# Performance work log

Measured on AMD Instinct MI355X. Metric: run time of the kernel, lower is better.

The kernel has to match this reference:

```python
import jax, jax.numpy as jnp
import numpy as np

B, S, I, H, C = 256, 128, 512, 1024, 10
VOCAB = S  # nn.Embedding(seq_length, input_dim)


def _lstm_dir(embeds_tbi, W, b):
    """Run an LSTM over time. embeds_tbi: [S,B,I]; W: [4H, I+H] stacked (g,i,f,o); b: [4H]."""
    h0 = jnp.zeros((B, H), jnp.float32)
    c0 = jnp.zeros((B, H), jnp.float32)

    def step(carry, x_t):
        c, h = carry
        xh = jnp.concatenate([x_t, h], axis=1)          # [B, I+H]
        z = xh @ W.T + b                                 # [B, 4H]
        g, i, f, o = jnp.split(z, 4, axis=1)
        g = jnp.tanh(g)
        i = jax.nn.sigmoid(i)
        f = jax.nn.sigmoid(f)
        o = jax.nn.sigmoid(o)
        new_c = g * i + c * f
        new_h = jnp.tanh(new_c) * o
        return (new_c, new_h), None

    (c_T, h_T), _ = jax.lax.scan(step, (c0, h0), embeds_tbi)
    return h_T


def setup_inputs() -> dict:
    key = jax.random.key(0)
    ks = jax.random.split(key, 8)
    x = jax.random.randint(ks[0], (B, S), 0, VOCAB)
    embed = jax.random.normal(ks[1], (VOCAB, I), jnp.float32) * 0.5
    scale = 1.0 / np.sqrt(I + H)
    fwd_W = jax.random.normal(ks[2], (4 * H, I + H), jnp.float32) * scale  # stacked g,i,f,o
    fwd_b = jax.random.normal(ks[3], (4 * H,), jnp.float32) * 0.02
    bwd_W = jax.random.normal(ks[4], (4 * H, I + H), jnp.float32) * scale
    bwd_b = jax.random.normal(ks[5], (4 * H,), jnp.float32) * 0.02
    p_w = jax.random.normal(ks[6], (C, 2 * H), jnp.float32) * (1.0 / np.sqrt(2 * H))
    p_b = jax.random.normal(ks[7], (C,), jnp.float32) * 0.02
    return {"x": x, "embed": embed, "fwd_W": fwd_W, "fwd_b": fwd_b,
            "bwd_W": bwd_W, "bwd_b": bwd_b, "p_w": p_w, "p_b": p_b}


def reference(x, embed, fwd_W, fwd_b, bwd_W, bwd_b, p_w, p_b):
    embeds = embed[x]                       # [B,S,I]
    emb_t = jnp.transpose(embeds, (1, 0, 2))  # [S,B,I]
    h_fwd = _lstm_dir(emb_t, fwd_W, fwd_b)
    h_bwd = _lstm_dir(emb_t[::-1], bwd_W, bwd_b)
    h_comb = jnp.concatenate([h_fwd, h_bwd], axis=1)  # [B,2H]
    return jax.nn.log_softmax(h_comb @ p_w.T + p_b, axis=1)
```

## Files before the change

### kernel.cpp

```cpp
#include <hip/hip_runtime.h>
#include <hip/hip_bf16.h>
#include <math.h>

#define B 256
#define S 128
#define I_DIM 512
#define H 1024
#define C 10
#define WROW 1536

#define LDS_H 131072

typedef float f32x4 __attribute__((ext_vector_type(4), may_alias));
typedef __bf16 bf16x8 __attribute__((ext_vector_type(8), may_alias));
typedef unsigned int u32x4 __attribute__((ext_vector_type(4), may_alias));
typedef unsigned long long u64;
typedef unsigned long long __attribute__((may_alias)) u64a;

__device__ __forceinline__ unsigned short f2bf(float f) {
    union { float f; unsigned u; } a; a.f = f;
    return (unsigned short)((a.u + 0x7fffu + ((a.u >> 16) & 1u)) >> 16);
}
__device__ __forceinline__ float bf2f(unsigned short b) {
    union { unsigned u; float f; } a; a.u = ((unsigned)b) << 16;
    return a.f;
}
__device__ __forceinline__ float sigf(float v) { return 1.0f / (1.0f + __expf(-v)); }
__device__ __forceinline__ float tanh_fast(float v) { return 1.0f - 2.0f / (1.0f + __expf(2.0f * v)); }

__global__ void wf_build(const float* __restrict__ fwd_W,
                         const float* __restrict__ bwd_W,
                         __hip_bfloat16* __restrict__ wF) {
    int gid = blockIdx.x * 256 + threadIdx.x;
    int lane = gid & 63, kk = (gid >> 6) & 31, nsub = (gid >> 11) & 255, d = gid >> 19;
    int n_gl = nsub * 16 + (lane & 15);
    int j = n_gl >> 2, g = n_gl & 3;
    int k = kk * 32 + (lane >> 4) * 8;
    const float* W = d ? bwd_W : fwd_W;
    const float* src = W + (size_t)(g * 1024 + j) * WROW + I_DIM + k;
    ushort4 lo = make_ushort4(f2bf(src[0]), f2bf(src[1]), f2bf(src[2]), f2bf(src[3]));
    ushort4 hi = make_ushort4(f2bf(src[4]), f2bf(src[5]), f2bf(src[6]), f2bf(src[7]));
    ushort4* dst = (ushort4*)(wF + (size_t)gid * 8);
    dst[0] = lo; dst[1] = hi;
}

__global__ void wxf_build(const float* __restrict__ fwd_W,
                          const float* __restrict__ bwd_W,
                          __hip_bfloat16* __restrict__ wxF) {
    int gid = blockIdx.x * 256 + threadIdx.x;
    int lane = gid & 63, kk = (gid >> 6) & 15, nsub = (gid >> 10) & 255, d = gid >> 18;
    int n_gl = nsub * 16 + (lane & 15);
    int j = n_gl >> 2, g = n_gl & 3;
    int k = kk * 32 + (lane >> 4) * 8;
    const float* W = d ? bwd_W : fwd_W;
    const float* src = W + (size_t)(g * 1024 + j) * WROW + k;
    ushort4 lo = make_ushort4(f2bf(src[0]), f2bf(src[1]), f2bf(src[2]), f2bf(src[3]));
    ushort4 hi = make_ushort4(f2bf(src[4]), f2bf(src[5]), f2bf(src[6]), f2bf(src[7]));
    ushort4* dst = (ushort4*)(wxF + (size_t)gid * 8);
    dst[0] = lo; dst[1] = hi;
}

__global__ void ehl_build(const float* __restrict__ embed,
                          unsigned short* __restrict__ ehl) {
    int idx = blockIdx.x * 256 + threadIdx.x;
    float e = embed[idx];
    unsigned short hb = f2bf(e);
    unsigned short lb = f2bf(e - bf2f(hb));
    ehl[idx] = hb;
    ehl[65536 + idx] = lb;
}

__global__ __launch_bounds__(256) void projp_mfma(
        const __hip_bfloat16* __restrict__ wxF,
        const unsigned short* __restrict__ ehl,
        const float* __restrict__ fwd_b,
        const float* __restrict__ bwd_b,
        float* __restrict__ projP) {
    extern __shared__ char sm[];
    const int bid = blockIdx.x;
    const int d = bid >> 7, jt = (bid >> 2) & 31, vb = bid & 3;
    const int tid = threadIdx.x, w = tid >> 6, lane = tid & 63;
    const int l15 = lane & 15, l4 = lane >> 4;
    const int v0 = vb * 32;

    for (int i = 0; i < 16; i++) {
        int chunk = i * 256 + tid;
        int row = chunk >> 6, c16 = chunk & 63;
        int p = row >> 5, vs = v0 + (row & 31);
        u32x4 vd = *(const u32x4*)(ehl + ((size_t)p * 128 + vs) * 512 + c16 * 8);
        *(u32x4*)(sm + row * 1024 + ((c16 * 16) ^ ((row & 7) << 4))) = vd;
    }
    __syncthreads();

    const __hip_bfloat16* ap0 = wxF + ((size_t)((d * 256 + jt * 8 + w * 2 + 0) * 16)) * 512;
    const __hip_bfloat16* ap1 = wxF + ((size_t)((d * 256 + jt * 8 + w * 2 + 1) * 16)) * 512;
    int hrow[2], hswz[2], lrow[2], lswz[2];
#pragma unroll
    for (int vt = 0; vt < 2; vt++) {
        int hr = vt * 16 + l15, lr = hr + 32;
        hrow[vt] = hr * 1024; hswz[vt] = (hr & 7) << 4;
        lrow[vt] = lr * 1024; lswz[vt] = (lr & 7) << 4;
    }
    f32x4 acc[2][2] = {};
#pragma unroll
    for (int kk = 0; kk < 16; kk++) {
        bf16x8 A0 = *(const bf16x8*)(ap0 + kk * 512 + lane * 8);
        bf16x8 A1 = *(const bf16x8*)(ap1 + kk * 512 + lane * 8);
        int ko = kk * 64 + l4 * 16;
        bf16x8 Bh0 = *(const bf16x8*)(sm + hrow[0] + (ko ^ hswz[0]));
        bf16x8 Bh1 = *(const bf16x8*)(sm + hrow[1] + (ko ^ hswz[1]));
        bf16x8 Bl0 = *(const bf16x8*)(sm + lrow[0] + (ko ^ lswz[0]));
        bf16x8 Bl1 = *(const bf16x8*)(sm + lrow[1] + (ko ^ lswz[1]));
        acc[0][0] = __builtin_amdgcn_mfma_f32_16x16x32_bf16(A0, Bh0, acc[0][0], 0, 0, 0);
        acc[0][0] = __builtin_amdgcn_mfma_f32_16x16x32_bf16(A0, Bl0, acc[0][0], 0, 0, 0);
        acc[0][1] = __builtin_amdgcn_mfma_f32_16x16x32_bf16(A0, Bh1, acc[0][1], 0, 0, 0);
        acc[0][1] = __builtin_amdgcn_mfma_f32_16x16x32_bf16(A0, Bl1, acc[0][1], 0, 0, 0);
        acc[1][0] = __builtin_amdgcn_mfma_f32_16x16x32_bf16(A1, Bh0, acc[1][0], 0, 0, 0);
        acc[1][0] = __builtin_amdgcn_mfma_f32_16x16x32_bf16(A1, Bl0, acc[1][0], 0, 0, 0);
        acc[1][1] = __builtin_amdgcn_mfma_f32_16x16x32_bf16(A1, Bh1, acc[1][1], 0, 0, 0);
        acc[1][1] = __builtin_amdgcn_mfma_f32_16x16x32_bf16(A1, Bl1, acc[1][1], 0, 0, 0);
    }
    const float* bp = d ? bwd_b : fwd_b;
#pragma unroll
    for (int nt = 0; nt < 2; nt++) {
        int j = jt * 32 + w * 8 + nt * 4 + l4;
        f32x4 bv = { bp[j], bp[1024 + j], bp[2048 + j], bp[3072 + j] };
#pragma unroll
        for (int vt = 0; vt < 2; vt++) {
            int v = v0 + vt * 16 + l15;
            *(f32x4*)(projP + ((size_t)(d * 1024 + j) * 128 + v) * 4) = acc[nt][vt] + bv;
        }
    }
}

__global__ __launch_bounds__(512, 1) void step_kernel(
        const int* __restrict__ x,
        const __hip_bfloat16* __restrict__ wF,
        const float* __restrict__ projP,
        __hip_bfloat16* __restrict__ hbuf,
        float* __restrict__ cws,
        int t) {
    extern __shared__ char smem[];
    const int bid = blockIdx.x;
    const int d = bid >> 7, bt = (bid >> 5) & 3, jt = bid & 31;
    const int tid = threadIdx.x, wid = tid >> 6, lane = tid & 63;
    const int l15 = lane & 15, l4 = lane >> 4;
    const int b0 = bt * 64;
    const size_t dBH = (size_t)d * B * H;

    const __hip_bfloat16* wp = wF + (size_t)(d * 256 + jt * 8 + wid) * 16384;

    bf16x8 Ap[8];
    if (t > 0) {
#pragma unroll
        for (int p = 0; p < 8; p++)
            Ap[p] = *(const bf16x8*)(wp + p * 512 + lane * 8);
    }
    const int tt = d ? (S - 1 - t) : t;
    int vv[4];
#pragma unroll
    for (int bs = 0; bs < 4; bs++)
        vv[bs] = x[(b0 + bs * 16 + l15) * S + tt];

    u32x4 sb1[8], sb2[8];
    int srow[8], sc16[8];
    if (t > 0) {
        const __hip_bfloat16* hr = hbuf + (size_t)(t & 1) * 2 * B * H + dBH + (size_t)b0 * H;
#pragma unroll
        for (int i = 0; i < 8; i++) {
            int flat = i * 512 + tid;
            srow[i] = flat >> 6;
            sc16[i] = flat & 63;
            sb1[i] = *(const u32x4*)(hr + (size_t)srow[i] * H + sc16[i] * 8);
        }
#pragma unroll
        for (int i = 0; i < 8; i++)
            sb2[i] = *(const u32x4*)(hr + (size_t)srow[i] * H + (sc16[i] + 64) * 8);
    }

    const int j = jt * 32 + wid * 4 + l4;
    const f32x4* pp = (const f32x4*)projP + ((size_t)d * 1024 + j) * 128;
    f32x4 pj[4];
#pragma unroll
    for (int bs = 0; bs < 4; bs++) pj[bs] = pp[vv[bs]];

    float* cp = cws + ((size_t)bid * 512 + tid) * 4;
    f32x4 cv = {0.f, 0.f, 0.f, 0.f};
    if (t > 0) cv = *(const f32x4*)cp;

    f32x4 acc[4] = {};
    if (t > 0) {
#pragma unroll
        for (int i = 0; i < 8; i++)
            *(u32x4*)(smem + srow[i] * 2048 + ((sc16[i] * 16) ^ ((srow[i] & 7) << 4))) = sb1[i];
        __syncthreads();

        int brow[4], bswz[4];
#pragma unroll
        for (int bs = 0; bs < 4; bs++) {
            int row = bs * 16 + l15;
            brow[bs] = row * 2048;
            bswz[bs] = (row & 7) << 4;
        }

#pragma unroll
        for (int kk = 0; kk < 16; kk++) {
            bf16x8 A = Ap[kk & 7];
            Ap[kk & 7] = *(const bf16x8*)(wp + (kk + 8) * 512 + lane * 8);
            int koff = kk * 64 + l4 * 16;
            bf16x8 B0 = *(const bf16x8*)(smem + brow[0] + (koff ^ bswz[0]));
            bf16x8 B1 = *(const bf16x8*)(smem + brow[1] + (koff ^ bswz[1]));
            bf16x8 B2 = *(const bf16x8*)(smem + brow[2] + (koff ^ bswz[2]));
            bf16x8 B3 = *(const bf16x8*)(smem + brow[3] + (koff ^ bswz[3]));
            acc[0] = __builtin_amdgcn_mfma_f32_16x16x32_bf16(A, B0, acc[0], 0, 0, 0);
            acc[1] = __builtin_amdgcn_mfma_f32_16x16x32_bf16(A, B1, acc[1], 0, 0, 0);
            acc[2] = __builtin_amdgcn_mfma_f32_16x16x32_bf16(A, B2, acc[2], 0, 0, 0);
            acc[3] = __builtin_amdgcn_mfma_f32_16x16x32_bf16(A, B3, acc[3], 0, 0, 0);
        }

#pragma unroll
        for (int i = 0; i < 8; i++)
            *(u32x4*)(smem + srow[i] * 2048 + (((sc16[i] + 64) * 16) ^ ((srow[i] & 7) << 4))) = sb2[i];
        __syncthreads();

#pragma unroll
        for (int kk = 16; kk < 32; kk++) {
            bf16x8 A = Ap[kk & 7];
            if (kk < 24)
                Ap[kk & 7] = *(const bf16x8*)(wp + (kk + 8) * 512 + lane * 8);
            int koff = kk * 64 + l4 * 16;
            bf16x8 B0 = *(const bf16x8*)(smem + brow[0] + (koff ^ bswz[0]));
            bf16x8 B1 = *(const bf16x8*)(smem + brow[1] + (koff ^ bswz[1]));
            bf16x8 B2 = *(const bf16x8*)(smem + brow[2] + (koff ^ bswz[2]));
            bf16x8 B3 = *(const bf16x8*)(smem + brow[3] + (koff ^ bswz[3]));
            acc[0] = __builtin_amdgcn_mfma_f32_16x16x32_bf16(A, B0, acc[0], 0, 0, 0);
            acc[1] = __builtin_amdgcn_mfma_f32_16x16x32_bf16(A, B1, acc[1], 0, 0, 0);
            acc[2] = __builtin_amdgcn_mfma_f32_16x16x32_bf16(A, B2, acc[2], 0, 0, 0);
            acc[3] = __builtin_amdgcn_mfma_f32_16x16x32_bf16(A, B3, acc[3], 0, 0, 0);
        }
    }

    float hnv[4];
#pragma unroll
    for (int bs = 0; bs < 4; bs++) {
        float zg = acc[bs][0] + pj[bs][0];
        float zi = acc[bs][1] + pj[bs][1];
        float zf = acc[bs][2] + pj[bs][2];
        float zo = acc[bs][3] + pj[bs][3];
        float gg = tanh_fast(zg);
        float ii = sigf(zi);
        float ff = sigf(zf);
        float oo = sigf(zo);
        float cn = gg * ii + cv[bs] * ff;
        cv[bs] = cn;
        hnv[bs] = tanh_fast(cn) * oo;
    }
    *(f32x4*)cp = cv;

    unsigned plo = (unsigned)f2bf(hnv[0]) | ((unsigned)f2bf(hnv[1]) << 16);
    unsigned phi = (unsigned)f2bf(hnv[2]) | ((unsigned)f2bf(hnv[3]) << 16);
    unsigned short o4[4];
#pragma unroll
    for (int p = 0; p < 4; p++) {
        int src = p * 16 + l15;
        unsigned vlo = __shfl(plo, src);
        unsigned vhi = __shfl(phi, src);
        unsigned sel = (l4 < 2) ? vlo : vhi;
        o4[p] = (l4 & 1) ? (unsigned short)(sel >> 16) : (unsigned short)(sel & 0xffffu);
    }
    u64 hv = (u64)o4[0] | ((u64)o4[1] << 16) | ((u64)o4[2] << 32) | ((u64)o4[3] << 48);
    __hip_bfloat16* hw = hbuf + (size_t)((t + 1) & 1) * 2 * B * H + dBH
                         + (size_t)(b0 + lane) * H + jt * 32 + wid * 4;
    *(u64a*)hw = hv;
}

__global__ void head_kernel(const __hip_bfloat16* __restrict__ hbuf,
                            const float* __restrict__ p_w,
                            const float* __restrict__ p_b,
                            float* __restrict__ out) {
    int b = blockIdx.x;
    int lane = threadIdx.x;
    float part[C];
#pragma unroll
    for (int cc = 0; cc < C; cc++) part[cc] = 0.0f;
    for (int jj = lane; jj < 2 * H; jj += 64) {
        float hv = (jj < H)
            ? __bfloat162float(hbuf[(size_t)b * H + jj])
            : __bfloat162float(hbuf[(size_t)B * H + (size_t)b * H + jj - H]);
#pragma unroll
        for (int cc = 0; cc < C; cc++) part[cc] += hv * p_w[cc * 2 * H + jj];
    }
#pragma unroll
    for (int cc = 0; cc < C; cc++) {
        float v = part[cc];
        for (int off = 32; off; off >>= 1) v += __shfl_down(v, off);
        part[cc] = v;
    }
    if (lane == 0) {
        float lg[C];
        float m = -1e30f;
        for (int cc = 0; cc < C; cc++) {
            lg[cc] = part[cc] + p_b[cc];
            m = fmaxf(m, lg[cc]);
        }
        float s = 0.0f;
        for (int cc = 0; cc < C; cc++) s += expf(lg[cc] - m);
        float lse = logf(s) + m;
        for (int cc = 0; cc < C; cc++) out[b * C + cc] = lg[cc] - lse;
    }
}

extern "C" void kernel_launch(void* const* d_in, const int* in_sizes, int n_in,
                              void* d_out, int out_size, void* d_ws, size_t ws_size,
                              hipStream_t stream) {
    const int*   x     = (const int*)d_in[0];
    const float* embed = (const float*)d_in[1];
    const float* fwd_W = (const float*)d_in[2];
    const float* fwd_b = (const float*)d_in[3];
    const float* bwd_W = (const float*)d_in[4];
    const float* bwd_b = (const float*)d_in[5];
    const float* p_w   = (const float*)d_in[6];
    const float* p_b   = (const float*)d_in[7];
    float* outp = (float*)d_out;

    char* ws = (char*)d_ws;
    __hip_bfloat16* wF  = (__hip_bfloat16*)ws;  ws += (size_t)2 * 256 * 16384 * 2;
    __hip_bfloat16* wxF = (__hip_bfloat16*)ws;
    float* cws = (float*)ws;                    ws += (size_t)2 * 256 * 8192 * 2;
    unsigned short* ehl = (unsigned short*)ws;  ws += (size_t)2 * 128 * 512 * 2;
    float* projP = (float*)ws;                  ws += (size_t)2 * 1024 * 128 * 4 * 4;
    __hip_bfloat16* hbuf = (__hip_bfloat16*)ws; ws += (size_t)2 * 2 * B * H * 2;

    hipLaunchKernelGGL(wf_build, dim3(4096), dim3(256), 0, stream, fwd_W, bwd_W, wF);
    hipLaunchKernelGGL(wxf_build, dim3(2048), dim3(256), 0, stream, fwd_W, bwd_W, wxF);
    hipLaunchKernelGGL(ehl_build, dim3(256), dim3(256), 0, stream, embed, ehl);

    hipFuncSetAttribute((const void*)projp_mfma,
                        hipFuncAttributeMaxDynamicSharedMemorySize, 65536);
    hipLaunchKernelGGL(projp_mfma, dim3(256), dim3(256), 65536, stream,
                       wxF, ehl, fwd_b, bwd_b, projP);

    hipFuncSetAttribute((const void*)step_kernel,
                        hipFuncAttributeMaxDynamicSharedMemorySize, LDS_H);
    for (int t = 0; t < S; t++)
        hipLaunchKernelGGL(step_kernel, dim3(256), dim3(512), LDS_H, stream,
                           x, wF, projP, hbuf, cws, t);

    hipLaunchKernelGGL(head_kernel, dim3(B), dim3(64), 0, stream,
                       hbuf, p_w, p_b, outp);
}
```

Baseline: 1.648 ms.

## Switch recurrent step to 32x32x16 MFMA with single-pass LDS staging

```diff
diff --git a/kernel.cpp b/kernel.cpp
--- a/kernel.cpp
+++ b/kernel.cpp
@@ -12,6 +12,7 @@
 #define LDS_H 131072
 
 typedef float f32x4 __attribute__((ext_vector_type(4), may_alias));
+typedef float f32x16 __attribute__((ext_vector_type(16), may_alias));
 typedef __bf16 bf16x8 __attribute__((ext_vector_type(8), may_alias));
 typedef unsigned int u32x4 __attribute__((ext_vector_type(4), may_alias));
 typedef unsigned long long u64;
@@ -28,14 +29,14 @@
 __device__ __forceinline__ float sigf(float v) { return 1.0f / (1.0f + __expf(-v)); }
 __device__ __forceinline__ float tanh_fast(float v) { return 1.0f - 2.0f / (1.0f + __expf(2.0f * v)); }
 
-__global__ void wf_build(const float* __restrict__ fwd_W,
-                         const float* __restrict__ bwd_W,
-                         __hip_bfloat16* __restrict__ wF) {
+__global__ void wf_build32(const float* __restrict__ fwd_W,
+                           const float* __restrict__ bwd_W,
+                           __hip_bfloat16* __restrict__ wF) {
     int gid = blockIdx.x * 256 + threadIdx.x;
-    int lane = gid & 63, kk = (gid >> 6) & 31, nsub = (gid >> 11) & 255, d = gid >> 19;
-    int n_gl = nsub * 16 + (lane & 15);
+    int lane = gid & 63, kstep = (gid >> 6) & 63, nsub = (gid >> 12) & 127, d = gid >> 19;
+    int n_gl = nsub * 32 + (lane & 31);
     int j = n_gl >> 2, g = n_gl & 3;
-    int k = kk * 32 + (lane >> 4) * 8;
+    int k = kstep * 16 + (lane >> 5) * 8;
     const float* W = d ? bwd_W : fwd_W;
     const float* src = W + (size_t)(g * 1024 + j) * WROW + I_DIM + k;
     ushort4 lo = make_ushort4(f2bf(src[0]), f2bf(src[1]), f2bf(src[2]), f2bf(src[3]));
@@ -144,11 +145,12 @@
     const int bid = blockIdx.x;
     const int d = bid >> 7, bt = (bid >> 5) & 3, jt = bid & 31;
     const int tid = threadIdx.x, wid = tid >> 6, lane = tid & 63;
-    const int l15 = lane & 15, l4 = lane >> 4;
+    const int ngrp = wid >> 1, bgrp = wid & 1;
+    const int l31 = lane & 31, l32 = lane >> 5;
     const int b0 = bt * 64;
     const size_t dBH = (size_t)d * B * H;
 
-    const __hip_bfloat16* wp = wF + (size_t)(d * 256 + jt * 8 + wid) * 16384;
+    const __hip_bfloat16* wp = wF + (size_t)(d * 128 + jt * 4 + ngrp) * 32768;
 
     bf16x8 Ap[8];
     if (t > 0) {
@@ -157,120 +159,79 @@
             Ap[p] = *(const bf16x8*)(wp + p * 512 + lane * 8);
     }
     const int tt = d ? (S - 1 - t) : t;
-    int vv[4];
-#pragma unroll
-    for (int bs = 0; bs < 4; bs++)
-        vv[bs] = x[(b0 + bs * 16 + l15) * S + tt];
-
-    u32x4 sb1[8], sb2[8];
-    int srow[8], sc16[8];
-    if (t > 0) {
-        const __hip_bfloat16* hr = hbuf + (size_t)(t & 1) * 2 * B * H + dBH + (size_t)b0 * H;
-#pragma unroll
-        for (int i = 0; i < 8; i++) {
-            int flat = i * 512 + tid;
-            srow[i] = flat >> 6;
-            sc16[i] = flat & 63;
-            sb1[i] = *(const u32x4*)(hr + (size_t)srow[i] * H + sc16[i] * 8);
-        }
-#pragma unroll
-        for (int i = 0; i < 8; i++)
-            sb2[i] = *(const u32x4*)(hr + (size_t)srow[i] * H + (sc16[i] + 64) * 8);
-    }
-
-    const int j = jt * 32 + wid * 4 + l4;
-    const f32x4* pp = (const f32x4*)projP + ((size_t)d * 1024 + j) * 128;
-    f32x4 pj[4];
-#pragma unroll
-    for (int bs = 0; bs < 4; bs++) pj[bs] = pp[vv[bs]];
+    const int bg = b0 + bgrp * 32 + l31;
+    const int vv = x[bg * S + tt];
 
     float* cp = cws + ((size_t)bid * 512 + tid) * 4;
     f32x4 cv = {0.f, 0.f, 0.f, 0.f};
     if (t > 0) cv = *(const f32x4*)cp;
 
-    f32x4 acc[4] = {};
     if (t > 0) {
-#pragma unroll
-        for (int i = 0; i < 8; i++)
-            *(u32x4*)(smem + srow[i] * 2048 + ((sc16[i] * 16) ^ ((srow[i] & 7) << 4))) = sb1[i];
+        const __hip_bfloat16* hr = hbuf + (size_t)(t & 1) * 2 * B * H + dBH + (size_t)b0 * H;
+#pragma unroll
+        for (int i = 0; i < 16; i++) {
+            int flat = i * 512 + tid;
+            int row = flat >> 7, c16 = flat & 127;
+            u32x4 v = *(const u32x4*)(hr + (size_t)row * H + c16 * 8);
+            *(u32x4*)(smem + row * 2048 + ((c16 * 16) ^ ((row & 7) << 4))) = v;
+        }
+    }
+
+    f32x4 pj[4];
+#pragma unroll
+    for (int p = 0; p < 4; p++) {
+        int j = jt * 32 + ngrp * 8 + 2 * p + l32;
+        pj[p] = *((const f32x4*)projP + ((size_t)(d * 1024 + j) * 128 + vv));
+    }
+
+    f32x16 acc = {};
+    if (t > 0) {
         __syncthreads();
-
-        int brow[4], bswz[4];
-#pragma unroll
-        for (int bs = 0; bs < 4; bs++) {
-            int row = bs * 16 + l15;
-            brow[bs] = row * 2048;
-            bswz[bs] = (row & 7) << 4;
+        const int brow = (bgrp * 32 + l31) * 2048;
+        const int bswz = (l31 & 7) << 4;
+        bf16x8 Bp[4];
+#pragma unroll
+        for (int p = 0; p < 4; p++)
+            Bp[p] = *(const bf16x8*)(smem + brow + ((p * 32 + l32 * 16) ^ bswz));
+#pragma unroll
+        for (int kk = 0; kk < 64; kk++) {
+            bf16x8 A = Ap[kk & 7];
+            bf16x8 Bv = Bp[kk & 3];
+            if (kk < 56)
+                Ap[kk & 7] = *(const bf16x8*)(wp + (kk + 8) * 512 + lane * 8);
+            if (kk < 60)
+                Bp[kk & 3] = *(const bf16x8*)(smem + brow + (((kk + 4) * 32 + l32 * 16) ^ bswz));
+            acc = __builtin_amdgcn_mfma_f32_32x32x16_bf16(A, Bv, acc, 0, 0, 0);
         }
-
-#pragma unroll
-        for (int kk = 0; kk < 16; kk++) {
-            bf16x8 A = Ap[kk & 7];
-            Ap[kk & 7] = *(const bf16x8*)(wp + (kk + 8) * 512 + lane * 8);
-            int koff = kk * 64 + l4 * 16;
-            bf16x8 B0 = *(const bf16x8*)(smem + brow[0] + (koff ^ bswz[0]));
-            bf16x8 B1 = *(const bf16x8*)(smem + brow[1] + (koff ^ bswz[1]));
-            bf16x8 B2 = *(const bf16x8*)(smem + brow[2] + (koff ^ bswz[2]));
-            bf16x8 B3 = *(const bf16x8*)(smem + brow[3] + (koff ^ bswz[3]));
-            acc[0] = __builtin_amdgcn_mfma_f32_16x16x32_bf16(A, B0, acc[0], 0, 0, 0);
-            acc[1] = __builtin_amdgcn_mfma_f32_16x16x32_bf16(A, B1, acc[1], 0, 0, 0);
-            acc[2] = __builtin_amdgcn_mfma_f32_16x16x32_bf16(A, B2, acc[2], 0, 0, 0);
-            acc[3] = __builtin_amdgcn_mfma_f32_16x16x32_bf16(A, B3, acc[3], 0, 0, 0);
-        }
-
-#pragma unroll
-        for (int i = 0; i < 8; i++)
-            *(u32x4*)(smem + srow[i] * 2048 + (((sc16[i] + 64) * 16) ^ ((srow[i] & 7) << 4))) = sb2[i];
-        __syncthreads();
-
-#pragma unroll
-        for (int kk = 16; kk < 32; kk++) {
-            bf16x8 A = Ap[kk & 7];
-            if (kk < 24)
-                Ap[kk & 7] = *(const bf16x8*)(wp + (kk + 8) * 512 + lane * 8);
-            int koff = kk * 64 + l4 * 16;
-            bf16x8 B0 = *(const bf16x8*)(smem + brow[0] + (koff ^ bswz[0]));
-            bf16x8 B1 = *(const bf16x8*)(smem + brow[1] + (koff ^ bswz[1]));
-            bf16x8 B2 = *(const bf16x8*)(smem + brow[2] + (koff ^ bswz[2]));
-            bf16x8 B3 = *(const bf16x8*)(smem + brow[3] + (koff ^ bswz[3]));
-            acc[0] = __builtin_amdgcn_mfma_f32_16x16x32_bf16(A, B0, acc[0], 0, 0, 0);
-            acc[1] = __builtin_amdgcn_mfma_f32_16x16x32_bf16(A, B1, acc[1], 0, 0, 0);
-            acc[2] = __builtin_amdgcn_mfma_f32_16x16x32_bf16(A, B2, acc[2], 0, 0, 0);
-            acc[3] = __builtin_amdgcn_mfma_f32_16x16x32_bf16(A, B3, acc[3], 0, 0, 0);
-        }
     }
 
     float hnv[4];
 #pragma unroll
-    for (int bs = 0; bs < 4; bs++) {
-        float zg = acc[bs][0] + pj[bs][0];
-        float zi = acc[bs][1] + pj[bs][1];
-        float zf = acc[bs][2] + pj[bs][2];
-        float zo = acc[bs][3] + pj[bs][3];
+    for (int p = 0; p < 4; p++) {
+        float zg = acc[4 * p + 0] + pj[p][0];
+        float zi = acc[4 * p + 1] + pj[p][1];
+        float zf = acc[4 * p + 2] + pj[p][2];
+        float zo = acc[4 * p + 3] + pj[p][3];
         float gg = tanh_fast(zg);
         float ii = sigf(zi);
         float ff = sigf(zf);
         float oo = sigf(zo);
-        float cn = gg * ii + cv[bs] * ff;
-        cv[bs] = cn;
-        hnv[bs] = tanh_fast(cn) * oo;
+        float cn = gg * ii + cv[p] * ff;
+        cv[p] = cn;
+        hnv[p] = tanh_fast(cn) * oo;
     }
     *(f32x4*)cp = cv;
 
-    unsigned plo = (unsigned)f2bf(hnv[0]) | ((unsigned)f2bf(hnv[1]) << 16);
-    unsigned phi = (unsigned)f2bf(hnv[2]) | ((unsigned)f2bf(hnv[3]) << 16);
-    unsigned short o4[4];
-#pragma unroll
-    for (int p = 0; p < 4; p++) {
-        int src = p * 16 + l15;
-        unsigned vlo = __shfl(plo, src);
-        unsigned vhi = __shfl(phi, src);
-        unsigned sel = (l4 < 2) ? vlo : vhi;
-        o4[p] = (l4 & 1) ? (unsigned short)(sel >> 16) : (unsigned short)(sel & 0xffffu);
-    }
-    u64 hv = (u64)o4[0] | ((u64)o4[1] << 16) | ((u64)o4[2] << 32) | ((u64)o4[3] << 48);
+    unsigned w0 = (unsigned)f2bf(hnv[0]) | ((unsigned)f2bf(hnv[1]) << 16);
+    unsigned w1 = (unsigned)f2bf(hnv[2]) | ((unsigned)f2bf(hnv[3]) << 16);
+    unsigned pw0 = __shfl(w0, lane ^ 32);
+    unsigned pw1 = __shfl(w1, lane ^ 32);
+    unsigned a  = l32 ? pw1 : w0;
+    unsigned b2 = l32 ? w1 : pw0;
+    u64 hv = (u64)(a & 0xffffu) | ((u64)(b2 & 0xffffu) << 16)
+           | ((u64)(a >> 16) << 32) | ((u64)(b2 >> 16) << 48);
     __hip_bfloat16* hw = hbuf + (size_t)((t + 1) & 1) * 2 * B * H + dBH
-                         + (size_t)(b0 + lane) * H + jt * 32 + wid * 4;
+                         + (size_t)bg * H + jt * 32 + ngrp * 8 + l32 * 4;
     *(u64a*)hw = hv;
 }
 
@@ -324,14 +285,14 @@
     float* outp = (float*)d_out;
 
     char* ws = (char*)d_ws;
-    __hip_bfloat16* wF  = (__hip_bfloat16*)ws;  ws += (size_t)2 * 256 * 16384 * 2;
+    __hip_bfloat16* wF  = (__hip_bfloat16*)ws;  ws += (size_t)2 * 128 * 64 * 64 * 8 * 2;
     __hip_bfloat16* wxF = (__hip_bfloat16*)ws;
     float* cws = (float*)ws;                    ws += (size_t)2 * 256 * 8192 * 2;
     unsigned short* ehl = (unsigned short*)ws;  ws += (size_t)2 * 128 * 512 * 2;
     float* projP = (float*)ws;                  ws += (size_t)2 * 1024 * 128 * 4 * 4;
     __hip_bfloat16* hbuf = (__hip_bfloat16*)ws; ws += (size_t)2 * 2 * B * H * 2;
 
-    hipLaunchKernelGGL(wf_build, dim3(4096), dim3(256), 0, stream, fwd_W, bwd_W, wF);
+    hipLaunchKernelGGL(wf_build32, dim3(4096), dim3(256), 0, stream, fwd_W, bwd_W, wF);
     hipLaunchKernelGGL(wxf_build, dim3(2048), dim3(256), 0, stream, fwd_W, bwd_W, wxF);
     hipLaunchKernelGGL(ehl_build, dim3(256), dim3(256), 0, stream, embed, ehl);
 
```

Measured after the change: 1.792 ms. +8.8%, slower.
